# Optimization experiments

Hardware: AMD Instinct MI355X
Metric: run time of the kernel (lower is better)

The kernel has to match this reference:

```python
import jax, jax.numpy as jnp
import numpy as np

HEADS = 4
BN_EPS = 1e-5


def setup_inputs() -> dict:
    key = jax.random.key(0)
    k1, k2, k3 = jax.random.split(key, 3)
    b, c, n = 4, 256, 4096
    x = jax.random.normal(k1, (b, c, n), dtype=jnp.float32)
    bn_weight = jnp.ones((c,), dtype=jnp.float32)
    bn_bias = jnp.zeros((c,), dtype=jnp.float32)
    # 1x1 Conv1d kernels are plain [out, in] matrices
    w_qkv = jax.random.normal(k2, (3 * c, c), dtype=jnp.float32) * (c ** -0.5)
    w_out = jax.random.normal(k3, (c, c), dtype=jnp.float32) * (c ** -0.5)
    b_out = jnp.zeros((c,), dtype=jnp.float32)
    return {"x": x, "bn_weight": bn_weight, "bn_bias": bn_bias,
            "w_qkv": w_qkv, "w_out": w_out, "b_out": b_out}


def reference(x, bn_weight, bn_bias, w_qkv, w_out, b_out):
    b, c, n = x.shape
    h = HEADS
    d = c // h
    scale = d ** -0.5

    # BatchNorm1d (training-mode batch statistics over batch and length dims)
    mean = jnp.mean(x, axis=(0, 2), keepdims=True)            # [1,c,1]
    var = jnp.var(x, axis=(0, 2), keepdims=True)
    xn = (x - mean) * jax.lax.rsqrt(var + BN_EPS)
    xn = xn * bn_weight[None, :, None] + bn_bias[None, :, None]

    # 1x1 conv QKV projection == matmul over channel dim
    qkv = jnp.einsum('oc,bcn->bon', w_qkv, xn)                # [b,3c,n]
    q, k, v = jnp.split(qkv, 3, axis=1)                       # each [b,c,n]
    # b (h d) n -> b h d n
    q = q.reshape(b, h, d, n) * scale
    k = k.reshape(b, h, d, n)
    v = v.reshape(b, h, d, n)

    attn = jax.nn.softmax(jnp.einsum('bhdi,bhdj->bhij', q, k), axis=-1)
    out = jnp.einsum('bhij,bhdj->bhid', attn, v)              # [b,h,n,d]
    # b h n d -> b (h d) n
    out = out.transpose(0, 1, 3, 2).reshape(b, c, n)
    return jnp.einsum('oc,bcn->bon', w_out, out) + b_out[None, :, None]
```

## Files before the change

### kernel.cpp

```cpp
#include <hip/hip_runtime.h>
#include <stdint.h>

#define B_ 4
#define C_ 256
#define N_ 4096
#define H_ 4
#define DH_ 64
#define BH_ 16

typedef __bf16 bf16x8 __attribute__((ext_vector_type(8)));
typedef __bf16 bf16x4 __attribute__((ext_vector_type(4)));
typedef float  f32x4  __attribute__((ext_vector_type(4)));
typedef float  f32x16 __attribute__((ext_vector_type(16)));
typedef unsigned short u16;

__device__ __forceinline__ u16 f2bf(float f) {
  uint32_t u = __float_as_uint(f);
  return (u16)((u + 0x7FFFu + ((u >> 16) & 1u)) >> 16);
}

__device__ __forceinline__ f32x4 mfma16(bf16x8 a, bf16x8 b, f32x4 c) {
  return __builtin_amdgcn_mfma_f32_16x16x32_bf16(a, b, c, 0, 0, 0);
}
__device__ __forceinline__ f32x16 mfma32(bf16x8 a, bf16x8 b, f32x16 c) {
  return __builtin_amdgcn_mfma_f32_32x32x16_bf16(a, b, c, 0, 0, 0);
}
__device__ __forceinline__ unsigned pk2(float a, float b) {
  unsigned r;
  asm("v_cvt_pk_bf16_f32 %0, %1, %2" : "=v"(r) : "v"(a), "v"(b));
  return r;
}

__global__ __launch_bounds__(256) void k_bnstats(const float* __restrict__ x,
    const float* __restrict__ bw, const float* __restrict__ bbias,
    float* __restrict__ a, float* __restrict__ bb) {
  int ch = blockIdx.x, t = threadIdx.x;
  float s1 = 0.f, s2 = 0.f;
  for (int b = 0; b < B_; ++b) {
    const float4* p = (const float4*)(x + ((size_t)b * C_ + ch) * N_);
    for (int i = t; i < N_ / 4; i += 256) {
      float4 v = p[i];
      s1 += v.x + v.y + v.z + v.w;
      s2 += v.x * v.x + v.y * v.y + v.z * v.z + v.w * v.w;
    }
  }
  for (int off = 32; off; off >>= 1) { s1 += __shfl_down(s1, off); s2 += __shfl_down(s2, off); }
  __shared__ float r1[4], r2[4];
  int w = t >> 6;
  if ((t & 63) == 0) { r1[w] = s1; r2[w] = s2; }
  __syncthreads();
  if (t == 0) {
    s1 = r1[0] + r1[1] + r1[2] + r1[3];
    s2 = r2[0] + r2[1] + r2[2] + r2[3];
    const float inv = 1.f / (B_ * N_);
    float mean = s1 * inv;
    float var  = s2 * inv - mean * mean;
    float av = bw[ch] * rsqrtf(var + 1e-5f);
    a[ch] = av;
    bb[ch] = bbias[ch] - mean * av;
  }
}

__global__ __launch_bounds__(256) void k_fold(const float* __restrict__ wq,
    const float* __restrict__ wo, const float* __restrict__ a, const float* __restrict__ bb,
    u16* __restrict__ wqf, float* __restrict__ qb, u16* __restrict__ woh) {
  int o = blockIdx.x, t = threadIdx.x;
  if (o < 3 * C_) {
    float w = wq[o * C_ + t];
    wqf[o * C_ + t] = f2bf(w * a[t]);
    float contrib = w * bb[t];
    for (int off = 32; off; off >>= 1) contrib += __shfl_down(contrib, off);
    __shared__ float r[4];
    if ((t & 63) == 0) r[t >> 6] = contrib;
    __syncthreads();
    if (t == 0) qb[o] = r[0] + r[1] + r[2] + r[3];
  } else {
    int oo = o - 3 * C_;
    woh[oo * C_ + t] = f2bf(wo[oo * C_ + t]);
  }
}

__global__ __launch_bounds__(256) void k_transpose(const float* __restrict__ x,
                                                   u16* __restrict__ xT) {
  __shared__ float tile[64][65];
  int nb = blockIdx.x * 64, cb = blockIdx.y * 64, b = blockIdx.z;
  int t = threadIdx.x;
  int col = t & 63, rq = t >> 6;
  #pragma unroll
  for (int it = 0; it < 16; ++it) {
    int r = it * 4 + rq;
    tile[r][col] = x[((size_t)b * C_ + cb + r) * N_ + nb + col];
  }
  __syncthreads();
  #pragma unroll
  for (int it = 0; it < 16; ++it) {
    int r = it * 4 + rq;
    xT[((size_t)b * N_ + nb + r) * C_ + cb + col] = f2bf(tile[col][r]);
  }
}

__global__ __launch_bounds__(256) void k_qkvgemm(const u16* __restrict__ xT,
    const u16* __restrict__ wqf, const float* __restrict__ qb,
    u16* __restrict__ q, u16* __restrict__ kk, u16* __restrict__ vtt) {
  __shared__ __align__(16) u16 As[128 * 64];
  __shared__ __align__(16) u16 Bs[128 * 64];
  int b = blockIdx.y;
  int bx = blockIdx.x;
  int mt = bx % 32, ot = bx / 32;
  int mbase = mt * 128, obase = ot * 128;
  int tid = threadIdx.x, w = tid >> 6, lane = tid & 63, lg = lane >> 4, lr = lane & 15;
  int wm = w >> 1, wn = w & 1;
  f32x4 acc[4][4] = {};
  const char* asrc = (const char*)xT + ((size_t)b * N_ + mbase) * 512;
  const char* bsrc = (const char*)wqf + (size_t)obase * 512;

  for (int ks = 0; ks < 4; ++ks) {
    int kbase = ks * 64;
    #pragma unroll
    for (int rr = 0; rr < 4; ++rr) {
      int p = tid * 16 + rr * 4096;
      int row = p >> 7, col = p & 127;
      int phys = p ^ ((row & 7) << 4);
      *(bf16x8*)((char*)As + phys) = *(const bf16x8*)(asrc + (size_t)row * 512 + kbase * 2 + col);
      *(bf16x8*)((char*)Bs + phys) = *(const bf16x8*)(bsrc + (size_t)row * 512 + kbase * 2 + col);
    }
    __syncthreads();
    #pragma unroll
    for (int kc = 0; kc < 2; ++kc) {
      bf16x8 af[4], bfr[4];
      #pragma unroll
      for (int i = 0; i < 4; ++i) {
        int r = wm * 64 + i * 16 + lr;
        int L = r * 128 + kc * 64 + lg * 16;
        af[i] = *(const bf16x8*)((const char*)As + (L ^ ((r & 7) << 4)));
        int rb = wn * 64 + i * 16 + lr;
        int Lb = rb * 128 + kc * 64 + lg * 16;
        bfr[i] = *(const bf16x8*)((const char*)Bs + (Lb ^ ((rb & 7) << 4)));
      }
      #pragma unroll
      for (int i = 0; i < 4; ++i)
        #pragma unroll
        for (int jj = 0; jj < 4; ++jj)
          acc[i][jj] = mfma16(af[i], bfr[jj], acc[i][jj]);
    }
    __syncthreads();
  }

  int s_id = (obase + wn * 64) >> 8;
  int h = ((obase + wn * 64) >> 6) & 3;
  int bh = b * H_ + h;
  float scale = (s_id == 0) ? 0.18033688011112042f : 1.f;
  #pragma unroll
  for (int i = 0; i < 4; ++i) {
    int n0 = mbase + wm * 64 + i * 16 + lg * 4;
    #pragma unroll
    for (int jj = 0; jj < 4; ++jj) {
      int o = obase + wn * 64 + jj * 16 + lr;
      int dd = jj * 16 + lr;
      float bias = qb[o];
      if (s_id == 2) {
        ushort4 pk;
        pk.x = f2bf(acc[i][jj][0] + bias);
        pk.y = f2bf(acc[i][jj][1] + bias);
        pk.z = f2bf(acc[i][jj][2] + bias);
        pk.w = f2bf(acc[i][jj][3] + bias);
        *(ushort4*)(vtt + ((size_t)bh * DH_ + dd) * N_ + n0) = pk;
      } else {
        u16* dst = (s_id == 0 ? q : kk) + (size_t)bh * N_ * DH_;
        #pragma unroll
        for (int r2 = 0; r2 < 4; ++r2)
          dst[(size_t)(n0 + r2) * DH_ + dd] = f2bf((acc[i][jj][r2] + bias) * scale);
      }
    }
  }
}

__device__ __forceinline__ void stage_tile(const char* kg_t, const char* vg_bh, int kt,
                                           char* kbuf, char* vbuf, int w, int lane) {
  #pragma unroll
  for (int i = 0; i < 2; ++i) {
    int poff = w * 2048 + i * 1024 + lane * 16;
    int L = poff ^ (((poff >> 7) & 7) << 4);
    __builtin_amdgcn_global_load_lds(
        (const __attribute__((address_space(1))) void*)(kg_t + (size_t)kt * 8192 + L),
        (__attribute__((address_space(3))) void*)(kbuf + w * 2048 + i * 1024), 16, 0, 0);
    int d = L >> 7, col = L & 127;
    __builtin_amdgcn_global_load_lds(
        (const __attribute__((address_space(1))) void*)(vg_bh + (size_t)d * 8192 + (size_t)kt * 128 + col),
        (__attribute__((address_space(3))) void*)(vbuf + w * 2048 + i * 1024), 16, 0, 0);
  }
}

__global__ __launch_bounds__(256, 2) void k_attn(const u16* __restrict__ q,
    const u16* __restrict__ k, const u16* __restrict__ vt, u16* __restrict__ ao) {
  __shared__ __align__(16) char kt_s[2][8192];
  __shared__ __align__(16) char vt_s[2][8192];
  int id = blockIdx.x;
  int xcd = id & 7, j = id >> 3;
  int bh = xcd * 2 + (j >> 5);
  int qbase = (j & 31) * 128;
  int tid = threadIdx.x, w = tid >> 6, lane = tid & 63;
  int l31 = lane & 31, hi = lane >> 5;

  const char* kg_t = (const char*)(k + (size_t)bh * N_ * DH_);
  const char* vg_bh = (const char*)(vt + (size_t)bh * DH_ * N_);

  bf16x8 bq[4];
  {
    const u16* qp = q + ((size_t)bh * N_ + qbase + w * 32 + l31) * DH_;
    #pragma unroll
    for (int cc = 0; cc < 4; ++cc)
      bq[cc] = *(const bf16x8*)(qp + cc * 16 + hi * 8);
  }

  f32x16 Oacc0, Oacc1;
  #pragma unroll
  for (int i = 0; i < 16; ++i) { Oacc0[i] = 0.f; Oacc1[i] = 0.f; }
  float m = -1e30f, l = 0.f;

  stage_tile(kg_t, vg_bh, 0, kt_s[0], vt_s[0], w, lane);
  int cur = 0;
  for (int kt = 0; kt < N_ / 64; ++kt) {
    __syncthreads();
    if (kt + 1 < N_ / 64)
      stage_tile(kg_t, vg_bh, kt + 1, kt_s[cur ^ 1], vt_s[cur ^ 1], w, lane);

    const char* kb = kt_s[cur];
    const char* vb = vt_s[cur];
    bf16x8 kf[2][4], vf[2][4];
    #pragma unroll
    for (int kt2 = 0; kt2 < 2; ++kt2) {
      int row = kt2 * 32 + l31; int sw = (row & 7) << 4; int rb = row * 128;
      #pragma unroll
      for (int cc = 0; cc < 4; ++cc)
        kf[kt2][cc] = *(const bf16x8*)(kb + ((rb + cc * 32 + hi * 16) ^ sw));
    }
    #pragma unroll
    for (int dt = 0; dt < 2; ++dt) {
      int row = dt * 32 + l31; int sw = (row & 7) << 4; int rb = row * 128;
      #pragma unroll
      for (int ks = 0; ks < 4; ++ks)
        vf[dt][ks] = *(const bf16x8*)(vb + ((rb + ks * 32 + hi * 16) ^ sw));
    }

    f32x16 s0, s1;
    #pragma unroll
    for (int i = 0; i < 16; ++i) { s0[i] = 0.f; s1[i] = 0.f; }
    __builtin_amdgcn_s_setprio(1);
    #pragma unroll
    for (int cc = 0; cc < 4; ++cc) {
      s0 = mfma32(kf[0][cc], bq[cc], s0);
      s1 = mfma32(kf[1][cc], bq[cc], s1);
    }
    __builtin_amdgcn_s_setprio(0);

    float m8[8];
    #pragma unroll
    for (int i = 0; i < 8; ++i)
      m8[i] = fmaxf(fmaxf(s0[i], s0[i + 8]), fmaxf(s1[i], s1[i + 8]));
    float ma = fmaxf(fmaxf(m8[0], m8[1]), fmaxf(m8[2], m8[3]));
    float mb = fmaxf(fmaxf(m8[4], m8[5]), fmaxf(m8[6], m8[7]));
    float mxloc = fmaxf(ma, mb);

    if (!__all(mxloc <= m + 8.f)) {
      float mx = fmaxf(mxloc, __shfl_xor(mxloc, 32));
      float mn = fmaxf(m, mx);
      float al = __builtin_amdgcn_exp2f(m - mn);
      m = mn; l *= al;
      #pragma unroll
      for (int i = 0; i < 16; ++i) { Oacc0[i] *= al; Oacc1[i] *= al; }
    }

    #pragma unroll
    for (int i = 0; i < 16; ++i) {
      s0[i] = __builtin_amdgcn_exp2f(s0[i] - m);
      s1[i] = __builtin_amdgcn_exp2f(s1[i] - m);
    }
    float t8[8];
    #pragma unroll
    for (int i = 0; i < 8; ++i)
      t8[i] = (s0[i] + s0[i + 8]) + (s1[i] + s1[i + 8]);
    float sa = (t8[0] + t8[1]) + (t8[2] + t8[3]);
    float sb = (t8[4] + t8[5]) + (t8[6] + t8[7]);
    float sum = sa + sb;
    sum += __shfl_xor(sum, 32);
    l += sum;

    bf16x8 pa[4];
    #pragma unroll
    for (int ks = 0; ks < 4; ++ks) {
      const int a0 = 8 * (ks & 1);
      const f32x16& sv = (ks >> 1) ? s1 : s0;
      unsigned u0 = pk2(sv[a0 + 0], sv[a0 + 1]);
      unsigned u1 = pk2(sv[a0 + 2], sv[a0 + 3]);
      unsigned u2 = pk2(sv[a0 + 4], sv[a0 + 5]);
      unsigned u3 = pk2(sv[a0 + 6], sv[a0 + 7]);
      asm("v_permlane32_swap_b32 %0, %1" : "+v"(u0), "+v"(u2));
      asm("v_permlane32_swap_b32 %0, %1" : "+v"(u1), "+v"(u3));
      union { unsigned u[4]; bf16x8 b; } cv;
      cv.u[0] = u0; cv.u[1] = u1; cv.u[2] = u2; cv.u[3] = u3;
      pa[ks] = cv.b;
    }
    __builtin_amdgcn_s_setprio(1);
    #pragma unroll
    for (int ks = 0; ks < 4; ++ks) {
      Oacc0 = mfma32(vf[0][ks], pa[ks], Oacc0);
      Oacc1 = mfma32(vf[1][ks], pa[ks], Oacc1);
    }
    __builtin_amdgcn_s_setprio(0);
    cur ^= 1;
  }

  float rl = 1.f / l;
  size_t rowb = ((size_t)bh * N_ + qbase + w * 32 + l31) * DH_;
  #pragma unroll
  for (int dt = 0; dt < 2; ++dt) {
    const f32x16& O = dt ? Oacc1 : Oacc0;
    #pragma unroll
    for (int rq = 0; rq < 4; ++rq) {
      ushort4 pk4;
      pk4.x = f2bf(O[rq * 4 + 0] * rl);
      pk4.y = f2bf(O[rq * 4 + 1] * rl);
      pk4.z = f2bf(O[rq * 4 + 2] * rl);
      pk4.w = f2bf(O[rq * 4 + 3] * rl);
      *(ushort4*)(ao + rowb + dt * 32 + rq * 8 + hi * 4) = pk4;
    }
  }
}

__global__ __launch_bounds__(256) void k_outgemm(const u16* __restrict__ ao,
    const u16* __restrict__ woh, const float* __restrict__ b_out,
    float* __restrict__ out) {
  __shared__ __align__(16) u16 As[128 * 64];
  __shared__ __align__(16) u16 Bs[128 * 64];
  int b = blockIdx.y;
  int bx = blockIdx.x;
  int mt = bx & 31, ot = bx >> 5;
  int mbase = mt * 128, obase = ot * 128;
  int tid = threadIdx.x, w = tid >> 6, lane = tid & 63, lg = lane >> 4, lr = lane & 15;
  int wm = w >> 1, wn = w & 1;
  f32x4 acc[4][4] = {};
  const char* bsrc = (const char*)woh + (size_t)obase * 512;

  for (int ks = 0; ks < 4; ++ks) {
    int kbase = ks * 64;
    int h = kbase >> 6;
    const char* asrc = (const char*)ao + ((size_t)(b * H_ + h) * N_ + mbase) * 128;
    #pragma unroll
    for (int rr = 0; rr < 4; ++rr) {
      int p = tid * 16 + rr * 4096;
      int row = p >> 7, col = p & 127;
      int phys = p ^ ((row & 7) << 4);
      *(bf16x8*)((char*)As + phys) = *(const bf16x8*)(asrc + p);
      *(bf16x8*)((char*)Bs + phys) = *(const bf16x8*)(bsrc + (size_t)row * 512 + kbase * 2 + col);
    }
    __syncthreads();
    #pragma unroll
    for (int kc = 0; kc < 2; ++kc) {
      bf16x8 af[4], bfr[4];
      #pragma unroll
      for (int i = 0; i < 4; ++i) {
        int r = wm * 64 + i * 16 + lr;
        int L = r * 128 + kc * 64 + lg * 16;
        af[i] = *(const bf16x8*)((const char*)As + (L ^ ((r & 7) << 4)));
        int rb = wn * 64 + i * 16 + lr;
        int Lb = rb * 128 + kc * 64 + lg * 16;
        bfr[i] = *(const bf16x8*)((const char*)Bs + (Lb ^ ((rb & 7) << 4)));
      }
      #pragma unroll
      for (int i = 0; i < 4; ++i)
        #pragma unroll
        for (int jj = 0; jj < 4; ++jj)
          acc[i][jj] = mfma16(af[i], bfr[jj], acc[i][jj]);
    }
    __syncthreads();
  }

  #pragma unroll
  for (int i = 0; i < 4; ++i) {
    int n0 = mbase + wm * 64 + i * 16 + lg * 4;
    #pragma unroll
    for (int jj = 0; jj < 4; ++jj) {
      int o = obase + wn * 64 + jj * 16 + lr;
      float bias = b_out[o];
      float4 vv = make_float4(acc[i][jj][0] + bias, acc[i][jj][1] + bias,
                              acc[i][jj][2] + bias, acc[i][jj][3] + bias);
      *(float4*)(out + ((size_t)(b * C_ + o)) * N_ + n0) = vv;
    }
  }
}

extern "C" void kernel_launch(void* const* d_in, const int* in_sizes, int n_in,
                              void* d_out, int out_size, void* d_ws, size_t ws_size,
                              hipStream_t stream) {
  const float* x    = (const float*)d_in[0];
  const float* bnw  = (const float*)d_in[1];
  const float* bnb  = (const float*)d_in[2];
  const float* wqkv = (const float*)d_in[3];
  const float* wout = (const float*)d_in[4];
  const float* bout = (const float*)d_in[5];
  float* out = (float*)d_out;
  char* ws = (char*)d_ws;

  float* a   = (float*)(ws + 0);
  float* bb  = (float*)(ws + 1024);
  float* qb  = (float*)(ws + 2048);
  u16* wqf = (u16*)(ws + 8192);
  u16* woh = (u16*)(ws + 8192 + 393216);
  const size_t big = 8388608;
  u16* xT  = (u16*)(ws + 532480);
  u16* q   = (u16*)(ws + 532480 + 1 * big);
  u16* kk  = (u16*)(ws + 532480 + 2 * big);
  u16* vt  = (u16*)(ws + 532480 + 3 * big);
  u16* ao  = (u16*)(ws + 532480 + 4 * big);

  k_bnstats  <<<256, 256, 0, stream>>>(x, bnw, bnb, a, bb);
  k_fold     <<<1024, 256, 0, stream>>>(wqkv, wout, a, bb, wqf, qb, woh);
  k_transpose<<<dim3(64, 4, 4), 256, 0, stream>>>(x, xT);
  k_qkvgemm  <<<dim3(192, 4), 256, 0, stream>>>(xT, wqf, qb, q, kk, vt);
  k_attn     <<<dim3(512), 256, 0, stream>>>(q, kk, vt, ao);
  k_outgemm  <<<dim3(64, 4), 256, 0, stream>>>(ao, woh, bout, out);
}
```

Before: 141.1 us.

## Split attention over KV halves, fuse BN stats into transpose, MFMA row sums

BatchNorm statistics are now computed as partial sums inside the transpose kernel, which removes a separate full pass over x. The attention kernel splits the key sequence into two halves, doubling the grid to 1024 blocks, and raises the occupancy hint to 4. Each half writes a partial output plus a log-sum-exp, and a new combine kernel merges them. Inside the loop, the softmax row sum is computed with an extra MFMA against a ones vector, max3 is used for the row max, and V fragment loads are deferred until after QK. The cost is extra workspace traffic for the partial outputs and one more kernel launch, and buffers such as xT and ao are reused as scratch.

```diff
diff --git a/kernel.cpp b/kernel.cpp
--- a/kernel.cpp
+++ b/kernel.cpp
@@ -7,9 +7,9 @@
 #define H_ 4
 #define DH_ 64
 #define BH_ 16
+#define NTH 32
 
 typedef __bf16 bf16x8 __attribute__((ext_vector_type(8)));
-typedef __bf16 bf16x4 __attribute__((ext_vector_type(4)));
 typedef float  f32x4  __attribute__((ext_vector_type(4)));
 typedef float  f32x16 __attribute__((ext_vector_type(16)));
 typedef unsigned short u16;
@@ -18,7 +18,6 @@
   uint32_t u = __float_as_uint(f);
   return (u16)((u + 0x7FFFu + ((u >> 16) & 1u)) >> 16);
 }
-
 __device__ __forceinline__ f32x4 mfma16(bf16x8 a, bf16x8 b, f32x4 c) {
   return __builtin_amdgcn_mfma_f32_16x16x32_bf16(a, b, c, 0, 0, 0);
 }
@@ -30,24 +29,48 @@
   asm("v_cvt_pk_bf16_f32 %0, %1, %2" : "=v"(r) : "v"(a), "v"(b));
   return r;
 }
-
-__global__ __launch_bounds__(256) void k_bnstats(const float* __restrict__ x,
-    const float* __restrict__ bw, const float* __restrict__ bbias,
-    float* __restrict__ a, float* __restrict__ bb) {
+__device__ __forceinline__ float max3f(float a, float b, float c) {
+  float r;
+  asm("v_max3_f32 %0, %1, %2, %3" : "=v"(r) : "v"(a), "v"(b), "v"(c));
+  return r;
+}
+
+__global__ __launch_bounds__(256) void k_prep(const float* __restrict__ x,
+    u16* __restrict__ xT, float* __restrict__ s1p, float* __restrict__ s2p) {
+  __shared__ float tile[64][65];
+  int nbt = blockIdx.x, nb = nbt * 64, cb = blockIdx.y * 64, b = blockIdx.z;
+  int t = threadIdx.x, col = t & 63, rq = t >> 6;
+  int part = b * 64 + nbt;
+  #pragma unroll
+  for (int it = 0; it < 16; ++it) {
+    int r = it * 4 + rq;
+    float v = x[((size_t)b * C_ + cb + r) * N_ + nb + col];
+    tile[r][col] = v;
+    float s = v, sq = v * v;
+    #pragma unroll
+    for (int off = 32; off; off >>= 1) { s += __shfl_xor(s, off); sq += __shfl_xor(sq, off); }
+    if (col == 0) {
+      s1p[(size_t)(cb + r) * 256 + part] = s;
+      s2p[(size_t)(cb + r) * 256 + part] = sq;
+    }
+  }
+  __syncthreads();
+  #pragma unroll
+  for (int it = 0; it < 16; ++it) {
+    int r = it * 4 + rq;
+    xT[((size_t)b * N_ + nb + r) * C_ + cb + col] = f2bf(tile[col][r]);
+  }
+}
+
+__global__ __launch_bounds__(256) void k_bnfin(const float* __restrict__ s1p,
+    const float* __restrict__ s2p, const float* __restrict__ bw,
+    const float* __restrict__ bbias, float* __restrict__ a, float* __restrict__ bb) {
   int ch = blockIdx.x, t = threadIdx.x;
-  float s1 = 0.f, s2 = 0.f;
-  for (int b = 0; b < B_; ++b) {
-    const float4* p = (const float4*)(x + ((size_t)b * C_ + ch) * N_);
-    for (int i = t; i < N_ / 4; i += 256) {
-      float4 v = p[i];
-      s1 += v.x + v.y + v.z + v.w;
-      s2 += v.x * v.x + v.y * v.y + v.z * v.z + v.w * v.w;
-    }
-  }
-  for (int off = 32; off; off >>= 1) { s1 += __shfl_down(s1, off); s2 += __shfl_down(s2, off); }
+  float s1 = s1p[(size_t)ch * 256 + t];
+  float s2 = s2p[(size_t)ch * 256 + t];
+  for (int off = 32; off; off >>= 1) { s1 += __shfl_xor(s1, off); s2 += __shfl_xor(s2, off); }
   __shared__ float r1[4], r2[4];
-  int w = t >> 6;
-  if ((t & 63) == 0) { r1[w] = s1; r2[w] = s2; }
+  if ((t & 63) == 0) { r1[t >> 6] = s1; r2[t >> 6] = s2; }
   __syncthreads();
   if (t == 0) {
     s1 = r1[0] + r1[1] + r1[2] + r1[3];
@@ -77,25 +100,6 @@
   } else {
     int oo = o - 3 * C_;
     woh[oo * C_ + t] = f2bf(wo[oo * C_ + t]);
-  }
-}
-
-__global__ __launch_bounds__(256) void k_transpose(const float* __restrict__ x,
-                                                   u16* __restrict__ xT) {
-  __shared__ float tile[64][65];
-  int nb = blockIdx.x * 64, cb = blockIdx.y * 64, b = blockIdx.z;
-  int t = threadIdx.x;
-  int col = t & 63, rq = t >> 6;
-  #pragma unroll
-  for (int it = 0; it < 16; ++it) {
-    int r = it * 4 + rq;
-    tile[r][col] = x[((size_t)b * C_ + cb + r) * N_ + nb + col];
-  }
-  __syncthreads();
-  #pragma unroll
-  for (int it = 0; it < 16; ++it) {
-    int r = it * 4 + rq;
-    xT[((size_t)b * N_ + nb + r) * C_ + cb + col] = f2bf(tile[col][r]);
   }
 }
 
@@ -175,35 +179,34 @@
   }
 }
 
-__device__ __forceinline__ void stage_tile(const char* kg_t, const char* vg_bh, int kt,
-                                           char* kbuf, char* vbuf, int w, int lane) {
-  #pragma unroll
-  for (int i = 0; i < 2; ++i) {
-    int poff = w * 2048 + i * 1024 + lane * 16;
-    int L = poff ^ (((poff >> 7) & 7) << 4);
-    __builtin_amdgcn_global_load_lds(
-        (const __attribute__((address_space(1))) void*)(kg_t + (size_t)kt * 8192 + L),
-        (__attribute__((address_space(3))) void*)(kbuf + w * 2048 + i * 1024), 16, 0, 0);
-    int d = L >> 7, col = L & 127;
-    __builtin_amdgcn_global_load_lds(
-        (const __attribute__((address_space(1))) void*)(vg_bh + (size_t)d * 8192 + (size_t)kt * 128 + col),
-        (__attribute__((address_space(3))) void*)(vbuf + w * 2048 + i * 1024), 16, 0, 0);
-  }
-}
-
-__global__ __launch_bounds__(256, 2) void k_attn(const u16* __restrict__ q,
-    const u16* __restrict__ k, const u16* __restrict__ vt, u16* __restrict__ ao) {
+#define AS1 __attribute__((address_space(1)))
+#define AS3 __attribute__((address_space(3)))
+
+__global__ __launch_bounds__(256, 4) void k_attn(const u16* __restrict__ q,
+    const u16* __restrict__ k, const u16* __restrict__ vt,
+    u16* __restrict__ O0, u16* __restrict__ O1, float* __restrict__ lse) {
   __shared__ __align__(16) char kt_s[2][8192];
   __shared__ __align__(16) char vt_s[2][8192];
   int id = blockIdx.x;
   int xcd = id & 7, j = id >> 3;
-  int bh = xcd * 2 + (j >> 5);
-  int qbase = (j & 31) * 128;
+  int bh = xcd * 2 + (j >> 6);
+  int rem = j & 63;
+  int qbase = (rem >> 1) * 128;
+  int half = rem & 1;
   int tid = threadIdx.x, w = tid >> 6, lane = tid & 63;
   int l31 = lane & 31, hi = lane >> 5;
 
-  const char* kg_t = (const char*)(k + (size_t)bh * N_ * DH_);
-  const char* vg_bh = (const char*)(vt + (size_t)bh * DH_ * N_);
+  const char* kg = (const char*)(k + ((size_t)bh * N_ + half * 2048) * DH_);
+  const char* vg = (const char*)(vt + (size_t)bh * DH_ * N_ + half * 2048);
+
+  int poff0 = w * 2048 + lane * 16;
+  int poff1 = poff0 + 1024;
+  int L0 = poff0 ^ (((poff0 >> 7) & 7) << 4);
+  int L1 = poff1 ^ (((poff1 >> 7) & 7) << 4);
+  const char* ks0 = kg + L0;
+  const char* ks1 = kg + L1;
+  const char* vs0 = vg + (size_t)(L0 >> 7) * 8192 + (L0 & 127);
+  const char* vs1 = vg + (size_t)(L1 >> 7) * 8192 + (L1 & 127);
 
   bf16x8 bq[4];
   {
@@ -212,22 +215,38 @@
     for (int cc = 0; cc < 4; ++cc)
       bq[cc] = *(const bf16x8*)(qp + cc * 16 + hi * 8);
   }
-
-  f32x16 Oacc0, Oacc1;
-  #pragma unroll
-  for (int i = 0; i < 16; ++i) { Oacc0[i] = 0.f; Oacc1[i] = 0.f; }
-  float m = -1e30f, l = 0.f;
-
-  stage_tile(kg_t, vg_bh, 0, kt_s[0], vt_s[0], w, lane);
-  int cur = 0;
-  for (int kt = 0; kt < N_ / 64; ++kt) {
-    __syncthreads();
-    if (kt + 1 < N_ / 64)
-      stage_tile(kg_t, vg_bh, kt + 1, kt_s[cur ^ 1], vt_s[cur ^ 1], w, lane);
-
-    const char* kb = kt_s[cur];
-    const char* vb = vt_s[cur];
-    bf16x8 kf[2][4], vf[2][4];
+  bf16x8 onesf;
+  {
+    union { u16 u[8]; bf16x8 b; } o;
+    #pragma unroll
+    for (int i = 0; i < 8; ++i) o.u[i] = 0x3F80;
+    onesf = o.b;
+  }
+
+  f32x16 Oacc0, Oacc1, lacc;
+  #pragma unroll
+  for (int i = 0; i < 16; ++i) { Oacc0[i] = 0.f; Oacc1[i] = 0.f; lacc[i] = 0.f; }
+  float m = -1e30f;
+
+  auto stage = [&](int par) {
+    __builtin_amdgcn_global_load_lds((const AS1 void*)ks0,
+        (AS3 void*)(kt_s[par] + w * 2048), 16, 0, 0);
+    __builtin_amdgcn_global_load_lds((const AS1 void*)ks1,
+        (AS3 void*)(kt_s[par] + w * 2048 + 1024), 16, 0, 0);
+    __builtin_amdgcn_global_load_lds((const AS1 void*)vs0,
+        (AS3 void*)(vt_s[par] + w * 2048), 16, 0, 0);
+    __builtin_amdgcn_global_load_lds((const AS1 void*)vs1,
+        (AS3 void*)(vt_s[par] + w * 2048 + 1024), 16, 0, 0);
+    ks0 += 8192; ks1 += 8192; vs0 += 128; vs1 += 128;
+  };
+
+  auto body = [&](int kt, int par) {
+    __syncthreads();
+    if (kt + 1 < NTH) stage(par ^ 1);
+
+    const char* kb = (const char*)kt_s[par];
+    const char* vb = (const char*)vt_s[par];
+    bf16x8 kf[2][4];
     #pragma unroll
     for (int kt2 = 0; kt2 < 2; ++kt2) {
       int row = kt2 * 32 + l31; int sw = (row & 7) << 4; int rb = row * 128;
@@ -235,14 +254,6 @@
       for (int cc = 0; cc < 4; ++cc)
         kf[kt2][cc] = *(const bf16x8*)(kb + ((rb + cc * 32 + hi * 16) ^ sw));
     }
-    #pragma unroll
-    for (int dt = 0; dt < 2; ++dt) {
-      int row = dt * 32 + l31; int sw = (row & 7) << 4; int rb = row * 128;
-      #pragma unroll
-      for (int ks = 0; ks < 4; ++ks)
-        vf[dt][ks] = *(const bf16x8*)(vb + ((rb + ks * 32 + hi * 16) ^ sw));
-    }
-
     f32x16 s0, s1;
     #pragma unroll
     for (int i = 0; i < 16; ++i) { s0[i] = 0.f; s1[i] = 0.f; }
@@ -254,39 +265,40 @@
     }
     __builtin_amdgcn_s_setprio(0);
 
-    float m8[8];
+    bf16x8 vf[2][4];
+    #pragma unroll
+    for (int dt = 0; dt < 2; ++dt) {
+      int row = dt * 32 + l31; int sw = (row & 7) << 4; int rb = row * 128;
+      #pragma unroll
+      for (int ks = 0; ks < 4; ++ks)
+        vf[dt][ks] = *(const bf16x8*)(vb + ((rb + ks * 32 + hi * 16) ^ sw));
+    }
+
+    float t8[8];
     #pragma unroll
     for (int i = 0; i < 8; ++i)
-      m8[i] = fmaxf(fmaxf(s0[i], s0[i + 8]), fmaxf(s1[i], s1[i + 8]));
-    float ma = fmaxf(fmaxf(m8[0], m8[1]), fmaxf(m8[2], m8[3]));
-    float mb = fmaxf(fmaxf(m8[4], m8[5]), fmaxf(m8[6], m8[7]));
-    float mxloc = fmaxf(ma, mb);
+      t8[i] = max3f(s0[i], s0[i + 8], fmaxf(s1[i], s1[i + 8]));
+    float m1 = max3f(t8[0], t8[1], t8[2]);
+    float m2 = max3f(t8[3], t8[4], t8[5]);
+    float mxloc = max3f(m1, m2, fmaxf(t8[6], t8[7]));
 
     if (!__all(mxloc <= m + 8.f)) {
       float mx = fmaxf(mxloc, __shfl_xor(mxloc, 32));
       float mn = fmaxf(m, mx);
       float al = __builtin_amdgcn_exp2f(m - mn);
-      m = mn; l *= al;
-      #pragma unroll
-      for (int i = 0; i < 16; ++i) { Oacc0[i] *= al; Oacc1[i] *= al; }
-    }
-
+      m = mn;
+      #pragma unroll
+      for (int i = 0; i < 16; ++i) {
+        Oacc0[i] *= al; Oacc1[i] *= al; lacc[i] *= al;
+      }
+    }
     #pragma unroll
     for (int i = 0; i < 16; ++i) {
       s0[i] = __builtin_amdgcn_exp2f(s0[i] - m);
       s1[i] = __builtin_amdgcn_exp2f(s1[i] - m);
     }
-    float t8[8];
-    #pragma unroll
-    for (int i = 0; i < 8; ++i)
-      t8[i] = (s0[i] + s0[i + 8]) + (s1[i] + s1[i + 8]);
-    float sa = (t8[0] + t8[1]) + (t8[2] + t8[3]);
-    float sb = (t8[4] + t8[5]) + (t8[6] + t8[7]);
-    float sum = sa + sb;
-    sum += __shfl_xor(sum, 32);
-    l += sum;
-
-    bf16x8 pa[4];
+
+    __builtin_amdgcn_s_setprio(1);
     #pragma unroll
     for (int ks = 0; ks < 4; ++ks) {
       const int a0 = 8 * (ks & 1);
@@ -299,20 +311,25 @@
       asm("v_permlane32_swap_b32 %0, %1" : "+v"(u1), "+v"(u3));
       union { unsigned u[4]; bf16x8 b; } cv;
       cv.u[0] = u0; cv.u[1] = u1; cv.u[2] = u2; cv.u[3] = u3;
-      pa[ks] = cv.b;
-    }
-    __builtin_amdgcn_s_setprio(1);
-    #pragma unroll
-    for (int ks = 0; ks < 4; ++ks) {
-      Oacc0 = mfma32(vf[0][ks], pa[ks], Oacc0);
-      Oacc1 = mfma32(vf[1][ks], pa[ks], Oacc1);
+      bf16x8 pa = cv.b;
+      Oacc0 = mfma32(vf[0][ks], pa, Oacc0);
+      Oacc1 = mfma32(vf[1][ks], pa, Oacc1);
+      lacc  = mfma32(onesf,     pa, lacc);
     }
     __builtin_amdgcn_s_setprio(0);
-    cur ^= 1;
-  }
-
+  };
+
+  stage(0);
+  for (int kt = 0; kt < NTH; kt += 2) {
+    body(kt, 0);
+    body(kt + 1, 1);
+  }
+
+  float l = lacc[0];
   float rl = 1.f / l;
-  size_t rowb = ((size_t)bh * N_ + qbase + w * 32 + l31) * DH_;
+  float lse_v = m + __builtin_amdgcn_logf(l);
+  int qrow = qbase + w * 32 + l31;
+  u16* dst = (half ? O1 : O0) + ((size_t)bh * N_ + qrow) * DH_;
   #pragma unroll
   for (int dt = 0; dt < 2; ++dt) {
     const f32x16& O = dt ? Oacc1 : Oacc0;
@@ -323,9 +340,33 @@
       pk4.y = f2bf(O[rq * 4 + 1] * rl);
       pk4.z = f2bf(O[rq * 4 + 2] * rl);
       pk4.w = f2bf(O[rq * 4 + 3] * rl);
-      *(ushort4*)(ao + rowb + dt * 32 + rq * 8 + hi * 4) = pk4;
-    }
-  }
+      *(ushort4*)(dst + dt * 32 + rq * 8 + hi * 4) = pk4;
+    }
+  }
+  if (hi == 0) lse[half * (BH_ * N_) + bh * N_ + qrow] = lse_v;
+}
+
+__global__ __launch_bounds__(256) void k_comb(const u16* __restrict__ O0,
+    const u16* __restrict__ O1, const float* __restrict__ lse, u16* __restrict__ dst) {
+  int t = blockIdx.x * 256 + threadIdx.x;
+  int row = t >> 3, dp = (t & 7) * 8;
+  float l0 = lse[row], l1 = lse[BH_ * N_ + row];
+  float M = fmaxf(l0, l1);
+  float w0 = __builtin_amdgcn_exp2f(l0 - M);
+  float w1 = __builtin_amdgcn_exp2f(l1 - M);
+  float inv = 1.f / (w0 + w1);
+  w0 *= inv; w1 *= inv;
+  uint4 a = *(const uint4*)(O0 + (size_t)row * 64 + dp);
+  uint4 b = *(const uint4*)(O1 + (size_t)row * 64 + dp);
+  uint4 o;
+  #pragma unroll
+  for (int i = 0; i < 4; ++i) {
+    unsigned ua = (&a.x)[i], ub = (&b.x)[i];
+    float alo = __uint_as_float(ua << 16), ahi = __uint_as_float(ua & 0xFFFF0000u);
+    float blo = __uint_as_float(ub << 16), bhi = __uint_as_float(ub & 0xFFFF0000u);
+    (&o.x)[i] = pk2(w0 * alo + w1 * blo, w0 * ahi + w1 * bhi);
+  }
+  *(uint4*)(dst + (size_t)row * 64 + dp) = o;
 }
 
 __global__ __launch_bounds__(256) void k_outgemm(const u16* __restrict__ ao,
@@ -413,11 +454,16 @@
   u16* kk  = (u16*)(ws + 532480 + 2 * big);
   u16* vt  = (u16*)(ws + 532480 + 3 * big);
   u16* ao  = (u16*)(ws + 532480 + 4 * big);
-
-  k_bnstats  <<<256, 256, 0, stream>>>(x, bnw, bnb, a, bb);
-  k_fold     <<<1024, 256, 0, stream>>>(wqkv, wout, a, bb, wqf, qb, woh);
-  k_transpose<<<dim3(64, 4, 4), 256, 0, stream>>>(x, xT);
-  k_qkvgemm  <<<dim3(192, 4), 256, 0, stream>>>(xT, wqf, qb, q, kk, vt);
-  k_attn     <<<dim3(512), 256, 0, stream>>>(q, kk, vt, ao);
-  k_outgemm  <<<dim3(64, 4), 256, 0, stream>>>(ao, woh, bout, out);
-}
+  const size_t tail = 532480 + 5 * big;
+  float* s1p = (float*)(ws + tail);
+  float* s2p = (float*)(ws + tail + 262144);
+  float* lse = (float*)(ws + tail);
+
+  k_prep   <<<dim3(64, 4, 4), 256, 0, stream>>>(x, xT, s1p, s2p);
+  k_bnfin  <<<256, 256, 0, stream>>>(s1p, s2p, bnw, bnb, a, bb);
+  k_fold   <<<1024, 256, 0, stream>>>(wqkv, wout, a, bb, wqf, qb, woh);
+  k_qkvgemm<<<dim3(192, 4), 256, 0, stream>>>(xT, wqf, qb, q, kk, vt);
+  k_attn   <<<dim3(1024), 256, 0, stream>>>(q, kk, vt, ao, xT, lse);
+  k_comb   <<<dim3(2048), 256, 0, stream>>>(ao, xT, lse, ao);
+  k_outgemm<<<dim3(64, 4), 256, 0, stream>>>(ao, woh, bout, out);
+}
```

New measurement: 286.2 us. 2.03x slower.
